# Kernel tuning notes

Hardware: AMD Instinct MI355X
Metric: run time of the kernel (lower is better)

The kernel has to match this reference:

```python
import jax, jax.numpy as jnp
import numpy as np
from jax import lax


def setup_inputs() -> dict:
    key = jax.random.key(0)
    ks = jax.random.split(key, 9)
    B = 4096
    x = jax.random.normal(ks[0], (B, 1, 28, 28), jnp.float32)

    def init(k, shape, fan_in):
        return (jax.random.normal(k, shape, jnp.float32) / np.float32(np.sqrt(fan_in)))

    W1 = init(ks[1], (32, 1, 3, 3), 1 * 9)
    b1 = init(ks[2], (32,), 1 * 9)
    W2 = init(ks[3], (64, 32, 3, 3), 32 * 9)
    b2 = init(ks[4], (64,), 32 * 9)
    Wl1 = init(ks[5], (14 * 14 * 64, 128), 14 * 14 * 64)
    bl1 = init(ks[6], (128,), 14 * 14 * 64)
    Wl2 = init(ks[7], (128, 10), 128)
    bl2 = init(ks[8], (10,), 128)
    return {"x": x, "W1": W1, "b1": b1, "W2": W2, "b2": b2,
            "Wl1": Wl1, "bl1": bl1, "Wl2": Wl2, "bl2": bl2}


def _conv_same(h, W, b):
    # submanifold sparse conv == SAME-padded dense conv, output restricted to active sites
    y = lax.conv_general_dilated(h, W, window_strides=(1, 1), padding="SAME",
                                 dimension_numbers=("NCHW", "OIHW", "NCHW"))
    return y + b[None, :, None, None]


def reference(x, W1, b1, W2, b2, Wl1, bl1, Wl2, bl2):
    # active-site mask from Voxels.from_dense (nonzero pixels); submanifold convs keep it fixed
    mask = (jnp.abs(x) > 0).any(axis=1, keepdims=True).astype(x.dtype)  # [B,1,28,28]
    h = jax.nn.relu(_conv_same(x, W1, b1) * mask)   # [B,32,28,28]
    h = jax.nn.relu(_conv_same(h, W2, b2) * mask)   # [B,64,28,28]
    # sparse 2x2/2 max pool; inactive sites are 0 and post-ReLU actives are >=0,
    # so dense window max == sparse max, and all-inactive windows densify to 0
    B = h.shape[0]
    h = h.reshape(B, 64, 14, 2, 14, 2).max(axis=(3, 5))  # [B,64,14,14]
    h = h.reshape(B, 64 * 14 * 14)
    # dropout is identity in eval
    h = jax.nn.relu(h @ Wl1 + bl1)
    logits = h @ Wl2 + bl2
    return jax.nn.log_softmax(logits, axis=1)
```

## Files before the change

kernel.cpp:

```cpp
#include <hip/hip_runtime.h>
#include <math.h>

typedef __bf16 bf16;
typedef __bf16 bf16x8 __attribute__((ext_vector_type(8)));
typedef unsigned short u16;
typedef unsigned short u16x4 __attribute__((ext_vector_type(4)));
typedef unsigned short u16x8 __attribute__((ext_vector_type(8)));
typedef float f32x4 __attribute__((ext_vector_type(4)));
typedef float f32x16 __attribute__((ext_vector_type(16)));
typedef unsigned int u32x4 __attribute__((ext_vector_type(4)));

__device__ __forceinline__ void load_lds16(const void* g, void* l) {
    __builtin_amdgcn_global_load_lds(
        (const __attribute__((address_space(1))) unsigned int*)g,
        (__attribute__((address_space(3))) unsigned int*)l, 16, 0, 0);
}

__global__ void prep_w2(const float* __restrict__ W2, bf16* __restrict__ w2r,
                        const float* __restrict__ W1, bf16* __restrict__ w1f) {
    int e = blockIdx.x * 256 + threadIdx.x;
    if (e < 18432) {
        int j  = e & 7;
        int l  = (e >> 3) & 63;
        int f  = e >> 9;
        int s  = f >> 1;
        int nt = f & 1;
        int tap  = s >> 1;
        int ci   = (s & 1) * 16 + (l >> 5) * 8 + j;
        int cout = nt * 32 + (l & 31);
        w2r[e] = (bf16)W2[cout * 288 + ci * 9 + tap];
    } else {
        int e2 = e - 18432;
        if (e2 < 512) {
            int j = e2 & 7;
            int l = e2 >> 3;
            int k = (l >> 5) * 8 + j;
            int n = l & 31;
            w1f[e2] = (k < 9) ? (bf16)W1[n * 9 + k] : (bf16)0.f;
        }
    }
}

__global__ void prep_wl1t(const float* __restrict__ Wl1, bf16* __restrict__ wl1t) {
    __shared__ float tile[32 * 129];
    const int t  = threadIdx.x;
    const int s  = blockIdx.x;
    const int cg = blockIdx.y;
    for (int e = t; e < 4096; e += 256) {
        int cl = e >> 7, n = e & 127;
        tile[cl * 129 + n] = Wl1[((long)(cg * 32 + cl) * 196 + s) * 128 + n];
    }
    __syncthreads();
    for (int e = t; e < 4096; e += 256) {
        int n = e >> 5, cl = e & 31;
        wl1t[(long)n * 12544 + s * 64 + cg * 32 + cl] = (bf16)tile[cl * 129 + n];
    }
}

__global__ __launch_bounds__(256, 3)
void conv_fused(const float* __restrict__ x, const float* __restrict__ b1,
                const bf16* __restrict__ w2r, const bf16* __restrict__ w1f,
                const float* __restrict__ b2, bf16* __restrict__ pooled)
{
    __shared__ __attribute__((aligned(16))) bf16  h1s[16 * 1032];
    __shared__ __attribute__((aligned(16))) bf16  Aim[512 * 16];
    __shared__ __attribute__((aligned(16))) u16   mrow[512];
    __shared__ __attribute__((aligned(16))) float mneg[98 * 4];
    __shared__ __attribute__((aligned(16))) bf16  xs[640];

    const int t    = threadIdx.x;
    const int lane = t & 63;
    const int wv   = t >> 6;
    const int img  = blockIdx.x >> 1;
    const int hb   = blockIdx.x & 1;
    const int nt   = wv & 1;
    const int wp   = wv >> 1;
    const int ml31 = lane & 31;
    const int lg   = lane >> 5;

    const float* xi = x + img * 784;

    bf16x8 breg[18];
    {
        const bf16x8* wp2 = (const bf16x8*)w2r;
        #pragma unroll
        for (int s = 0; s < 18; s++)
            breg[s] = wp2[(2 * s + nt) * 64 + lane];
    }
    const bf16x8 w1frag = *(const bf16x8*)&w1f[lane * 8];
    const float  b1r    = b1[ml31];
    const float  bias2  = b2[nt * 32 + ml31];

    for (int e = t; e < 640; e += 256) {
        int j  = e >> 5;
        int c  = e & 31;
        int xr = hb * 14 - 2 + j;
        int xc = c - 1;
        float v = 0.f;
        if (xr >= 0 && xr < 28 && xc >= 0 && xc < 28) v = xi[xr * 28 + xc];
        xs[e] = (bf16)v;
    }
    __syncthreads();

    const u16* xu = (const u16*)xs;
    #pragma unroll
    for (int pp = 0; pp < 2; pp++) {
        int p = t + pp * 256;
        int r = p >> 5, c = p & 31;
        int b = r * 32 + c - 1;
        u16 v0 = xu[b],      v1 = xu[b + 1],  v2 = xu[b + 2];
        u16 v3 = xu[b + 32], v4 = xu[b + 33], v5 = xu[b + 34];
        u16 v6 = xu[b + 64], v7 = xu[b + 65], v8 = xu[b + 66];
        u16x8 t0;
        t0[0] = v0; t0[1] = v1; t0[2] = v2; t0[3] = v3;
        t0[4] = v4; t0[5] = v5; t0[6] = v6; t0[7] = v7;
        u16x8 t1;
        #pragma unroll
        for (int j = 0; j < 8; j++) t1[j] = 0;
        t1[0] = v8;
        *(u16x8*)&Aim[p * 16]     = *(u16x8*)&t0;
        *(u16x8*)&Aim[p * 16 + 8] = *(u16x8*)&t1;
        mrow[p] = (c >= 1 && c <= 28 && (v4 & 0x7fff) != 0) ? 1 : 0;
    }
    for (int e = t; e < 392; e += 256) {
        int s   = e >> 2, q = e & 3;
        int spi = s / 14, spj = s - spi * 14;
        u16 cv = xu[(2 * spi + (q >> 1) + 2) * 32 + 2 * spj + (q & 1) + 1];
        mneg[e] = ((cv & 0x7fff) != 0) ? 0.f : -1e30f;
    }
    __syncthreads();

    for (int Mt = wv; Mt < 16; Mt += 4) {
        int m = Mt * 32 + ml31;
        bf16x8 af = *(const bf16x8*)&Aim[m * 16 + lg * 8];
        f32x16 acc;
        #pragma unroll
        for (int e = 0; e < 16; e++) acc[e] = b1r;
        acc = __builtin_amdgcn_mfma_f32_32x32x16_bf16(af, w1frag, acc, 0, 0, 0);
        const int rowb = Mt * 1032;
        #pragma unroll
        for (int run = 0; run < 4; run++) {
            int p0 = Mt * 32 + run * 8 + 4 * lg;
            u16x4 mk = *(const u16x4*)&mrow[p0];
            #pragma unroll
            for (int j = 0; j < 4; j++) {
                float s = acc[run * 4 + j];
                float o = (mk[j] != 0) ? fmaxf(s, 0.f) : 0.f;
                int col = run * 8 + 4 * lg + j;
                int swz = (col & 6) << 2;
                h1s[rowb + col * 32 + (ml31 ^ swz)] = (bf16)o;
            }
        }
    }
    __syncthreads();

    const int half = lg;
    const int cib  = half * 8;

    int q  = ml31 & 3;
    int pj = wp * 8 + (ml31 >> 2);
    int pi = 0;
    if (pj >= 14) { pj -= 14; pi = 1; }

    bf16* pout = pooled + (long)img * 12544 + hb * 98 * 64 + nt * 32 + ml31;

    for (int Mt = wp; Mt < 13; Mt += 2) {
        int row = 2 * pi + (q >> 1);
        if (row > 13) row = 13;
        int colb = 2 * pj + (q & 1);
        int rowb = row * 1032;

        int e0a[3], e1a[3];
        #pragma unroll
        for (int dc = 0; dc < 3; dc++) {
            int cc   = colb + dc;
            int swz  = (cc & 6) << 2;
            int base = rowb + cc * 32;
            e0a[dc] = base + (cib ^ swz);
            e1a[dc] = base + ((16 + cib) ^ swz);
        }

        f32x16 accA, accB = {};
        #pragma unroll
        for (int e = 0; e < 16; e++) accA[e] = bias2;

        #pragma unroll
        for (int dr = 0; dr < 3; dr++) {
            #pragma unroll
            for (int dc = 0; dc < 3; dc++) {
                const int tap = dr * 3 + dc;
                bf16x8 a0 = *(const bf16x8*)&h1s[e0a[dc] + dr * 1032];
                bf16x8 a1 = *(const bf16x8*)&h1s[e1a[dc] + dr * 1032];
                accA = __builtin_amdgcn_mfma_f32_32x32x16_bf16(a0, breg[2 * tap],     accA, 0, 0, 0);
                accB = __builtin_amdgcn_mfma_f32_32x32x16_bf16(a1, breg[2 * tap + 1], accB, 0, 0, 0);
            }
        }

        int slg = 8 * Mt + half;
        #pragma unroll
        for (int gg = 0; gg < 4; gg++) {
            if (slg < 98) {
                f32x4 mn = *(const f32x4*)&mneg[slg * 4];
                float v0 = accA[gg * 4 + 0] + accB[gg * 4 + 0] + mn[0];
                float v1 = accA[gg * 4 + 1] + accB[gg * 4 + 1] + mn[1];
                float v2 = accA[gg * 4 + 2] + accB[gg * 4 + 2] + mn[2];
                float v3 = accA[gg * 4 + 3] + accB[gg * 4 + 3] + mn[3];
                float pm = fmaxf(fmaxf(v0, v1), fmaxf(v2, v3));
                pout[slg * 64] = (bf16)fmaxf(pm, 0.f);
            }
            slg += 2;
        }

        pj += 2; if (pj >= 14) { pj -= 14; pi += 1; }
        pi += 1;
    }
}

__global__ __launch_bounds__(256, 4)
void fc1(const bf16* __restrict__ pooled, const bf16* __restrict__ wl1t,
         float* __restrict__ part)
{
    __shared__ __attribute__((aligned(16))) bf16 As[2][32 * 64];
    __shared__ __attribute__((aligned(16))) bf16 Bs[2][128 * 64];

    const int t    = threadIdx.x;
    const int lane = t & 63;
    const int wv   = t >> 6;
    const int ml   = lane & 15;
    const int kg   = lane >> 4;
    const int wm   = wv & 1;
    const int wn   = wv >> 1;
    const int m0   = blockIdx.x * 32;
    const int ks   = blockIdx.y;
    const int k0   = ks * 1792;

    const bf16* asrc;
    {
        int c  = t;
        int sub = c >> 7, i = c & 127;
        int r  = i >> 2;
        int jq = (i & 3) ^ ((r >> 1) & 3);
        asrc = pooled + (long)(m0 + r) * 12544 + k0 + sub * 32 + jq * 8;
    }
    bf16* adst0 = &As[0][wv * 512];
    bf16* adst1 = &As[1][wv * 512];

    const bf16* bsrc[4];
    int bbase[4];
    #pragma unroll
    for (int u = 0; u < 4; u++) {
        int c  = u * 256 + t;
        int sub = c >> 9, i = c & 511;
        int r  = i >> 2;
        int jq = (i & 3) ^ ((r >> 1) & 3);
        bsrc[u]  = wl1t + (long)r * 12544 + k0 + sub * 32 + jq * 8;
        bbase[u] = (u * 256 + wv * 64) * 8;
    }

    const int am = wm * 16 + ml;
    int aoff[2], boff[4];
    #pragma unroll
    for (int s = 0; s < 2; s++)
        aoff[s] = s * 1024 + ((am * 32 + kg * 8) ^ ((am & 6) << 2));
    #pragma unroll
    for (int j = 0; j < 4; j++) {
        int n = wn * 64 + j * 16 + ml;
        boff[j] = (n * 32 + kg * 8) ^ ((n & 6) << 2);
    }

    f32x4 acc[4];
    {
        f32x4 z = {0.f, 0.f, 0.f, 0.f};
        #pragma unroll
        for (int j = 0; j < 4; j++) acc[j] = z;
    }

    load_lds16(asrc, adst0);
    #pragma unroll
    for (int u = 0; u < 4; u++) load_lds16(bsrc[u], &Bs[0][bbase[u]]);

    for (int kt = 0; kt < 28; kt++) {
        __syncthreads();
        const int cur = kt & 1;
        if (kt < 27) {
            const int kb = (kt + 1) * 64;
            load_lds16(asrc + kb, cur ? adst0 : adst1);
            #pragma unroll
            for (int u = 0; u < 4; u++)
                load_lds16(bsrc[u] + kb, &Bs[cur ^ 1][bbase[u]]);
        }
        #pragma unroll
        for (int s = 0; s < 2; s++) {
            bf16x8 af = *(const bf16x8*)&As[cur][aoff[s]];
            #pragma unroll
            for (int j = 0; j < 4; j++) {
                bf16x8 bf = *(const bf16x8*)&Bs[cur][s * 4096 + boff[j]];
                acc[j] = __builtin_amdgcn_mfma_f32_16x16x32_bf16(af, bf, acc[j], 0, 0, 0);
            }
        }
    }

    float* pp = part + ((long)ks * 4096 + m0 + wm * 16) * 128 + wn * 64;
    #pragma unroll
    for (int j = 0; j < 4; j++)
        #pragma unroll
        for (int r = 0; r < 4; r++)
            pp[(kg * 4 + r) * 128 + j * 16 + ml] = acc[j][r];
}

__global__ __launch_bounds__(256)
void fc2_lsm(const float* __restrict__ part, const float* __restrict__ bl1,
             const float* __restrict__ Wl2, const float* __restrict__ bl2,
             float* __restrict__ out)
{
    const int wv   = threadIdx.x >> 6;
    const int lane = threadIdx.x & 63;
    const int img  = blockIdx.x * 4 + wv;
    const float* pb = part + (long)img * 128;

    float ac[10];
    #pragma unroll
    for (int c = 0; c < 10; c++) ac[c] = 0.f;

    #pragma unroll
    for (int u = 0; u < 2; u++) {
        int n = lane + 64 * u;
        float s = bl1[n];
        #pragma unroll
        for (int k = 0; k < 7; k++) s += pb[(long)k * 4096 * 128 + n];
        float h = s > 0.f ? s : 0.f;
        #pragma unroll
        for (int c = 0; c < 10; c++) ac[c] += h * Wl2[n * 10 + c];
    }
    #pragma unroll
    for (int o = 32; o > 0; o >>= 1)
        #pragma unroll
        for (int c = 0; c < 10; c++) ac[c] += __shfl_down(ac[c], o, 64);

    if (lane == 0) {
        float lg[10], mx = -1e30f;
        #pragma unroll
        for (int c = 0; c < 10; c++) {
            lg[c] = ac[c] + bl2[c];
            mx = lg[c] > mx ? lg[c] : mx;
        }
        float se = 0.f;
        #pragma unroll
        for (int c = 0; c < 10; c++) se += __expf(lg[c] - mx);
        float ls = __logf(se);
        #pragma unroll
        for (int c = 0; c < 10; c++) out[img * 10 + c] = lg[c] - mx - ls;
    }
}

extern "C" void kernel_launch(void* const* d_in, const int* in_sizes, int n_in,
                              void* d_out, int out_size, void* d_ws, size_t ws_size,
                              hipStream_t stream) {
    const float* x   = (const float*)d_in[0];
    const float* W1  = (const float*)d_in[1];
    const float* b1  = (const float*)d_in[2];
    const float* W2  = (const float*)d_in[3];
    const float* b2  = (const float*)d_in[4];
    const float* Wl1 = (const float*)d_in[5];
    const float* bl1 = (const float*)d_in[6];
    const float* Wl2 = (const float*)d_in[7];
    const float* bl2 = (const float*)d_in[8];
    float* out = (float*)d_out;

    char* ws = (char*)d_ws;
    bf16*  w2r    = (bf16*)ws;
    bf16*  w1f    = (bf16*)(ws + 40960);
    bf16*  wl1t   = (bf16*)(ws + 65536);
    bf16*  pooled = (bf16*)(ws + 65536 + 4194304);
    float* part   = (float*)(ws + 65536 + 4194304 + 102760448);

    prep_w2   <<<74,             256, 0, stream>>>(W2, w2r, W1, w1f);
    prep_wl1t <<<dim3(196, 2),   256, 0, stream>>>(Wl1, wl1t);
    conv_fused<<<8192,           256, 0, stream>>>(x, b1, w2r, w1f, b2, pooled);
    fc1       <<<dim3(128, 7),   256, 0, stream>>>(pooled, wl1t, part);
    fc2_lsm   <<<1024,           256, 0, stream>>>(part, bl1, Wl2, bl2, out);
}
```

Measured before the change: 268.5 us.

## Merge weight prep kernels and stage fc1 tiles through registers

Combines the two weight-preparation kernels into one launch, with block index deciding whether a block transposes Wl1 or reorders W2/W1, which removes one kernel launch. In fc1, replaces direct global-to-LDS async loads with register-staged loads: the next tile is fetched into registers before the MFMA loop and written to the other LDS buffer after it. This overlaps global latency with compute using ordinary loads, at the cost of more VGPRs and extra LDS write instructions.

```diff
diff --git a/kernel.cpp b/kernel.cpp
--- a/kernel.cpp
+++ b/kernel.cpp
@@ -10,50 +10,46 @@
 typedef float f32x16 __attribute__((ext_vector_type(16)));
 typedef unsigned int u32x4 __attribute__((ext_vector_type(4)));
 
-__device__ __forceinline__ void load_lds16(const void* g, void* l) {
-    __builtin_amdgcn_global_load_lds(
-        (const __attribute__((address_space(1))) unsigned int*)g,
-        (__attribute__((address_space(3))) unsigned int*)l, 16, 0, 0);
-}
-
-__global__ void prep_w2(const float* __restrict__ W2, bf16* __restrict__ w2r,
-                        const float* __restrict__ W1, bf16* __restrict__ w1f) {
-    int e = blockIdx.x * 256 + threadIdx.x;
-    if (e < 18432) {
-        int j  = e & 7;
-        int l  = (e >> 3) & 63;
-        int f  = e >> 9;
-        int s  = f >> 1;
-        int nt = f & 1;
-        int tap  = s >> 1;
-        int ci   = (s & 1) * 16 + (l >> 5) * 8 + j;
-        int cout = nt * 32 + (l & 31);
-        w2r[e] = (bf16)W2[cout * 288 + ci * 9 + tap];
+__global__ void prep_all(const float* __restrict__ W2, bf16* __restrict__ w2r,
+                         const float* __restrict__ W1, bf16* __restrict__ w1f,
+                         const float* __restrict__ Wl1, bf16* __restrict__ wl1t) {
+    __shared__ float tile[32 * 129];
+    const int b = blockIdx.x;
+    const int t = threadIdx.x;
+    if (b < 392) {
+        const int s  = b >> 1;
+        const int cg = b & 1;
+        for (int e = t; e < 4096; e += 256) {
+            int cl = e >> 7, n = e & 127;
+            tile[cl * 129 + n] = Wl1[((long)(cg * 32 + cl) * 196 + s) * 128 + n];
+        }
+        __syncthreads();
+        for (int e = t; e < 4096; e += 256) {
+            int n = e >> 5, cl = e & 31;
+            wl1t[(long)n * 12544 + s * 64 + cg * 32 + cl] = (bf16)tile[cl * 129 + n];
+        }
     } else {
-        int e2 = e - 18432;
-        if (e2 < 512) {
-            int j = e2 & 7;
-            int l = e2 >> 3;
-            int k = (l >> 5) * 8 + j;
-            int n = l & 31;
-            w1f[e2] = (k < 9) ? (bf16)W1[n * 9 + k] : (bf16)0.f;
-        }
-    }
-}
-
-__global__ void prep_wl1t(const float* __restrict__ Wl1, bf16* __restrict__ wl1t) {
-    __shared__ float tile[32 * 129];
-    const int t  = threadIdx.x;
-    const int s  = blockIdx.x;
-    const int cg = blockIdx.y;
-    for (int e = t; e < 4096; e += 256) {
-        int cl = e >> 7, n = e & 127;
-        tile[cl * 129 + n] = Wl1[((long)(cg * 32 + cl) * 196 + s) * 128 + n];
-    }
-    __syncthreads();
-    for (int e = t; e < 4096; e += 256) {
-        int n = e >> 5, cl = e & 31;
-        wl1t[(long)n * 12544 + s * 64 + cg * 32 + cl] = (bf16)tile[cl * 129 + n];
+        int e = (b - 392) * 256 + t;
+        if (e < 18432) {
+            int j  = e & 7;
+            int l  = (e >> 3) & 63;
+            int f  = e >> 9;
+            int s  = f >> 1;
+            int nt = f & 1;
+            int tap  = s >> 1;
+            int ci   = (s & 1) * 16 + (l >> 5) * 8 + j;
+            int cout = nt * 32 + (l & 31);
+            w2r[e] = (bf16)W2[cout * 288 + ci * 9 + tap];
+        } else {
+            int e2 = e - 18432;
+            if (e2 < 512) {
+                int j = e2 & 7;
+                int l = e2 >> 3;
+                int k = (l >> 5) * 8 + j;
+                int n = l & 31;
+                w1f[e2] = (k < 9) ? (bf16)W1[n * 9 + k] : (bf16)0.f;
+            }
+        }
     }
 }
 
@@ -236,25 +232,19 @@
 
     const bf16* asrc;
     {
-        int c  = t;
-        int sub = c >> 7, i = c & 127;
+        int sub = t >> 7, i = t & 127;
         int r  = i >> 2;
         int jq = (i & 3) ^ ((r >> 1) & 3);
         asrc = pooled + (long)(m0 + r) * 12544 + k0 + sub * 32 + jq * 8;
     }
-    bf16* adst0 = &As[0][wv * 512];
-    bf16* adst1 = &As[1][wv * 512];
-
     const bf16* bsrc[4];
-    int bbase[4];
     #pragma unroll
     for (int u = 0; u < 4; u++) {
         int c  = u * 256 + t;
         int sub = c >> 9, i = c & 511;
         int r  = i >> 2;
         int jq = (i & 3) ^ ((r >> 1) & 3);
-        bsrc[u]  = wl1t + (long)r * 12544 + k0 + sub * 32 + jq * 8;
-        bbase[u] = (u * 256 + wv * 64) * 8;
+        bsrc[u] = wl1t + (long)r * 12544 + k0 + sub * 32 + jq * 8;
     }
 
     const int am = wm * 16 + ml;
@@ -275,19 +265,22 @@
         for (int j = 0; j < 4; j++) acc[j] = z;
     }
 
-    load_lds16(asrc, adst0);
-    #pragma unroll
-    for (int u = 0; u < 4; u++) load_lds16(bsrc[u], &Bs[0][bbase[u]]);
+    u32x4 ra = *(const u32x4*)asrc;
+    u32x4 rb[4];
+    #pragma unroll
+    for (int u = 0; u < 4; u++) rb[u] = *(const u32x4*)bsrc[u];
+    *(u32x4*)&As[0][t * 8] = ra;
+    #pragma unroll
+    for (int u = 0; u < 4; u++) *(u32x4*)&Bs[0][(u * 256 + t) * 8] = rb[u];
 
     for (int kt = 0; kt < 28; kt++) {
         __syncthreads();
         const int cur = kt & 1;
         if (kt < 27) {
             const int kb = (kt + 1) * 64;
-            load_lds16(asrc + kb, cur ? adst0 : adst1);
-            #pragma unroll
-            for (int u = 0; u < 4; u++)
-                load_lds16(bsrc[u] + kb, &Bs[cur ^ 1][bbase[u]]);
+            ra = *(const u32x4*)(asrc + kb);
+            #pragma unroll
+            for (int u = 0; u < 4; u++) rb[u] = *(const u32x4*)(bsrc[u] + kb);
         }
         #pragma unroll
         for (int s = 0; s < 2; s++) {
@@ -297,6 +290,12 @@
                 bf16x8 bf = *(const bf16x8*)&Bs[cur][s * 4096 + boff[j]];
                 acc[j] = __builtin_amdgcn_mfma_f32_16x16x32_bf16(af, bf, acc[j], 0, 0, 0);
             }
+        }
+        if (kt < 27) {
+            *(u32x4*)&As[cur ^ 1][t * 8] = ra;
+            #pragma unroll
+            for (int u = 0; u < 4; u++)
+                *(u32x4*)&Bs[cur ^ 1][(u * 256 + t) * 8] = rb[u];
         }
     }
 
@@ -374,8 +373,7 @@
     bf16*  pooled = (bf16*)(ws + 65536 + 4194304);
     float* part   = (float*)(ws + 65536 + 4194304 + 102760448);
 
-    prep_w2   <<<74,             256, 0, stream>>>(W2, w2r, W1, w1f);
-    prep_wl1t <<<dim3(196, 2),   256, 0, stream>>>(Wl1, wl1t);
+    prep_all  <<<466,            256, 0, stream>>>(W2, w2r, W1, w1f, Wl1, wl1t);
     conv_fused<<<8192,           256, 0, stream>>>(x, b1, w2r, w1f, b2, pooled);
     fc1       <<<dim3(128, 7),   256, 0, stream>>>(pooled, wl1t, part);
     fc2_lsm   <<<1024,           256, 0, stream>>>(part, bl1, Wl2, bl2, out);
```

After: 259.1 us. -3.5%, faster.
